# Performance work log

Hardware: AMD Instinct MI355X
Metric: run time of the kernel (lower is better)

## Reference

```python
import jax, jax.numpy as jnp
import numpy as np

KH, KW = 3, 3
PAD = 1
C_IN, C_OUT = 64, 128


def unfold(x, kh, kw, pad):
    # x: (B, C, H, W) -> (B, C, kh*kw, H*W), torch.nn.functional.unfold ordering
    B, C, H, W = x.shape
    xp = jnp.pad(x, ((0, 0), (0, 0), (pad, pad), (pad, pad)))
    patches = jnp.stack(
        [xp[:, :, i:i + H, j:j + W] for i in range(kh) for j in range(kw)],
        axis=2,
    )  # (B, C, K, H, W)
    return patches.reshape(B, C, kh * kw, H * W)


def setup_inputs() -> dict:
    key = jax.random.key(0)
    k1, k2, k3 = jax.random.split(key, 3)
    B, H, W = 8, 128, 128
    inp = jax.random.normal(k1, (B, C_IN, H, W), dtype=jnp.float32)
    g_buffer = jax.random.uniform(k2, (B, 2, H, W), dtype=jnp.float32)
    # weights param as in torch: (1, C*kh*kw, 1, out_channels), kaiming-uniform-ish
    wdepth = C_IN * KH * KW
    bound = float(np.sqrt(6.0 / wdepth))
    weights = jax.random.uniform(k3, (1, wdepth, 1, C_OUT), dtype=jnp.float32,
                                 minval=-bound, maxval=bound)
    bias = jnp.zeros((C_OUT,), dtype=jnp.float32)
    return {"input": inp, "g_buffer": g_buffer, "weights": weights, "bias": bias}


def reference(input, g_buffer, weights, bias):
    B, C, H, W = input.shape
    K = KH * KW
    L = H * W
    depth = 2.0 * (g_buffer[:, -1:, :, :] - 0.5)  # (B, 1, H, W)

    input_unf = unfold(input, KH, KW, PAD)          # (B, C, K, L)
    depth_unf = unfold(depth, KH, KW, PAD)          # (B, 1, K, L)

    # bilateral depth weighting
    dfeat = depth_unf - depth.reshape(B, 1, 1, L)   # (B, 1, K, L)
    dfeat = jnp.sum(dfeat * dfeat, axis=1)          # (B, K, L)
    wf = jnp.exp(-dfeat)
    wf = 9.0 * wf / jnp.sum(wf, axis=1, keepdims=True)  # (B, K, L)

    filt = input_unf * wf[:, None, :, :]            # (B, C, K, L)
    filt = filt.reshape(B, C * K, L)

    W2 = weights.reshape(C_OUT, C * K)              # raw reshape, matches torch .view
    out_unf = jnp.einsum('bkl,ok->bol', filt, W2)   # (B, C_OUT, L)
    out = out_unf.reshape(B, C_OUT, H, W) + bias[None, :, None, None]
    return out
```

## Files before the change

kernel.cpp:

```cpp
#include <hip/hip_runtime.h>
#include <hip/hip_bf16.h>
#include <stdint.h>

typedef _Float16 f16x8 __attribute__((ext_vector_type(8)));
typedef float    f32x4 __attribute__((ext_vector_type(4)));

#define CIN   64
#define COUT  128
#define HH    128
#define WW    128
#define BB    8

#define TROW  130
#define ROWBYTES (130 * 128)
#define TSIZE ((size_t)BB * TROW * ROWBYTES)


__global__ void prep_weights(const float* __restrict__ wflat, _Float16* __restrict__ bp) {
    int idx = blockIdx.x * 256 + threadIdx.x;
    if (idx >= 8 * 18 * 64 * 8) return;
    int j = idx & 7;
    int l = (idx >> 3) & 63;
    int s = (idx >> 9) % 18;
    int n = idx / (18 * 512);
    int o = n * 16 + (l & 15);
    int c = ((s & 1) << 5) + ((l >> 4) << 3) + j;
    int k = s >> 1;
    bp[idx] = (_Float16)wflat[o * 576 + c * 9 + k];
}

__global__ void zero_halo(_Float16* __restrict__ T) {
    int idx = blockIdx.x * 256 + threadIdx.x;
    if (idx >= 16 * 1040) return;
    int row = idx / 1040, c = idx - row * 1040;
    int b = row >> 1, yp = (row & 1) * 129;
    f16x8 z = {};
    *(f16x8*)((char*)T + (size_t)(b * TROW + yp) * ROWBYTES + c * 16) = z;
}

__global__ __launch_bounds__(256) void transpose_pass(const float* __restrict__ inp,
                                                      _Float16* __restrict__ T) {
    __shared__ float sT[64][129];
    const int b   = blockIdx.x >> 7;
    const int y   = blockIdx.x & 127;
    const int tid = threadIdx.x;

    const float* ib = inp + ((long)b * CIN * HH + y) * WW;
    const int xq = tid & 31, c8 = tid >> 5;
    #pragma unroll
    for (int i = 0; i < 8; ++i) {
        int c = c8 * 8 + i;
        float4 v = *(const float4*)(ib + (long)c * (HH * WW) + (xq << 2));
        *(float4*)&sT[c][xq << 2] = v;
    }
    __syncthreads();

    const int x  = tid & 127;
    const int ch = tid >> 7;
    char* rowp = (char*)T + (size_t)(b * TROW + y + 1) * ROWBYTES + (size_t)(x + 1) * 128;
    const int sw = (x + 1) & 7;
    for (int c0 = ch * 8; c0 < 64; c0 += 16) {
        f16x8 v;
        #pragma unroll
        for (int j = 0; j < 8; ++j) v[j] = (_Float16)sT[c0 + j][x];
        *(f16x8*)(rowp + (((c0 >> 3) ^ sw) << 4)) = v;
    }
    if (tid < 16) {
        char* basep = (char*)T + (size_t)(b * TROW + y + 1) * ROWBYTES
                    + ((tid >> 3) ? 129 * 128 : 0) + (tid & 7) * 16;
        f16x8 z = {};
        *(f16x8*)basep = z;
    }
}

__global__ __launch_bounds__(512, 2) void depthcnn_main(
    const _Float16* __restrict__ T, const float* __restrict__ gbuf,
    const float* __restrict__ bias, const _Float16* __restrict__ aprep,
    float* __restrict__ out)
{
    __shared__ __align__(1024) char sIn[4 * ROWBYTES];
    __shared__ _Float16 sWf[4][9][WW];

    const int b      = blockIdx.x >> 5;
    const int ystart = (blockIdx.x & 31) << 2;
    const int tid    = threadIdx.x;
    const int wave   = tid >> 6;
    const int lane   = tid & 63;
    const int oi     = wave >> 1;
    const int pi     = wave & 1;
    const int l15    = lane & 15;
    const int g4     = lane >> 4;
    const int pxbase = pi << 6;

    const char* Tb = (const char*)T + (size_t)b * TROW * ROWBYTES;

    #pragma unroll
    for (int i = 0; i < 3; ++i) {
        const int t = ystart + i;
        const char* src = Tb + (size_t)t * ROWBYTES;
        char* dst = sIn + (t & 3) * ROWBYTES;
        for (int c = tid; c < 1040; c += 512)
            __builtin_amdgcn_global_load_lds(
                (const __attribute__((address_space(1))) uint32_t*)(src + c * 16),
                (__attribute__((address_space(3))) uint32_t*)(dst + c * 16), 16, 0, 0);
    }

    {
        const int r = tid >> 7, x = tid & 127, y = ystart + r;
        const float* g = gbuf + ((size_t)b * 2 + 1) * (HH * WW);
        float dc = 2.f * (g[y * WW + x] - 0.5f);
        float e[9];
        float ssum = 0.f;
        #pragma unroll
        for (int k = 0; k < 9; ++k) {
            int yy = y + (k / 3) - 1;
            int xx = x + (k % 3) - 1;
            float dn = 0.f;
            if ((unsigned)yy < 128u && (unsigned)xx < 128u)
                dn = 2.f * (g[yy * WW + xx] - 0.5f);
            float df = dn - dc;
            float ek = __expf(-df * df);
            e[k] = ek;
            ssum += ek;
        }
        float sc = 9.f / ssum;
        #pragma unroll
        for (int k = 0; k < 9; ++k) sWf[r][k][x] = (_Float16)(e[k] * sc);
    }

    f16x8 afr[2][18];
    {
        const f16x8* ap = (const f16x8*)aprep;
        #pragma unroll
        for (int t2 = 0; t2 < 2; ++t2)
            #pragma unroll
            for (int s = 0; s < 18; ++s)
                afr[t2][s] = ap[(size_t)(((oi * 2 + t2) * 18) + s) * 64 + lane];
    }
    float bv[2][4];
    #pragma unroll
    for (int t2 = 0; t2 < 2; ++t2)
        #pragma unroll
        for (int r4 = 0; r4 < 4; ++r4)
            bv[t2][r4] = bias[(oi << 5) + (t2 << 4) + (g4 << 2) + r4];

    __syncthreads();

    float* ob0 = out + (size_t)b * COUT * HH * WW;

    #pragma unroll 1
    for (int r = 0; r < 4; ++r) {
        const int y = ystart + r;

        if (r < 3) {
            const int t = y + 3;
            const char* src = Tb + (size_t)t * ROWBYTES;
            char* dst = sIn + (t & 3) * ROWBYTES;
            for (int c = tid; c < 1040; c += 512)
                __builtin_amdgcn_global_load_lds(
                    (const __attribute__((address_space(1))) uint32_t*)(src + c * 16),
                    (__attribute__((address_space(3))) uint32_t*)(dst + c * 16), 16, 0, 0);
        }

        f32x4 acc[2][4];
        #pragma unroll
        for (int t2 = 0; t2 < 2; ++t2)
            #pragma unroll
            for (int pt = 0; pt < 4; ++pt)
                acc[t2][pt] = (f32x4){0.f, 0.f, 0.f, 0.f};

        #pragma unroll
        for (int s = 0; s < 18; ++s) {
            const int k  = s >> 1;
            const int ch = s & 1;
            const int dy = k / 3;
            const int dx = k - 3 * dy;
            const int slotbase = ((y + dy) & 3) * ROWBYTES;
            f16x8 bfrg[4];
            #pragma unroll
            for (int pt = 0; pt < 4; ++pt) {
                const int px = pxbase + (pt << 4) + l15;
                const int xp = px + dx;
                const int off = slotbase + (xp << 7) + ((((ch << 2) | g4) ^ (xp & 7)) << 4);
                f16x8 iv = *(const f16x8*)(sIn + off);
                _Float16 wh = sWf[r][k][px];
                f16x8 w8 = {wh, wh, wh, wh, wh, wh, wh, wh};
                bfrg[pt] = iv * w8;
            }
            #pragma unroll
            for (int t2 = 0; t2 < 2; ++t2)
                #pragma unroll
                for (int pt = 0; pt < 4; ++pt)
                    acc[t2][pt] = __builtin_amdgcn_mfma_f32_16x16x32_f16(
                        afr[t2][s], bfrg[pt], acc[t2][pt], 0, 0, 0);
        }

        __syncthreads();

        #pragma unroll
        for (int t2 = 0; t2 < 2; ++t2) {
            #pragma unroll
            for (int pt = 0; pt < 4; ++pt) {
                #pragma unroll
                for (int r4 = 0; r4 < 4; ++r4) {
                    const int o  = (oi << 5) + (t2 << 4) + (g4 << 2) + r4;
                    const int px = pxbase + (pt << 4) + l15;
                    ob0[(size_t)o * (HH * WW) + (size_t)y * WW + px] = acc[t2][pt][r4] + bv[t2][r4];
                }
            }
        }
    }
}

extern "C" void kernel_launch(void* const* d_in, const int* in_sizes, int n_in,
                              void* d_out, int out_size, void* d_ws, size_t ws_size,
                              hipStream_t stream) {
    const float* inp  = (const float*)d_in[0];
    const float* gbuf = (const float*)d_in[1];
    const float* wts  = (const float*)d_in[2];
    const float* bias = (const float*)d_in[3];

    _Float16* T  = (_Float16*)d_ws;
    _Float16* bp = (_Float16*)((char*)d_ws + TSIZE);

    hipLaunchKernelGGL(zero_halo, dim3(65), dim3(256), 0, stream, T);
    hipLaunchKernelGGL(transpose_pass, dim3(BB * HH), dim3(256), 0, stream, inp, T);
    hipLaunchKernelGGL(prep_weights, dim3(288), dim3(256), 0, stream, wts, bp);
    hipLaunchKernelGGL(depthcnn_main, dim3(256), dim3(512), 0, stream,
                       T, gbuf, bias, bp, (float*)d_out);
}
```

Baseline: 52.02 us.

## Preload all six input rows to LDS upfront and drop per-row barriers

All six halo rows a block needs are loaded into LDS in a single upfront batch, replacing the rotating four-slot ring that prefetched one row per iteration. This removes the per-iteration __syncthreads. The depth-weight table is re-laid out per pixel so each lane loads its nine weights once per row with a vector read instead of a scalar LDS read inside every MFMA step. The cost is more LDS per block and giving up the overlap of row loads with compute.

```diff
diff --git a/kernel.cpp b/kernel.cpp
--- a/kernel.cpp
+++ b/kernel.cpp
@@ -78,8 +78,8 @@
     const float* __restrict__ bias, const _Float16* __restrict__ aprep,
     float* __restrict__ out)
 {
-    __shared__ __align__(1024) char sIn[4 * ROWBYTES];
-    __shared__ _Float16 sWf[4][9][WW];
+    __shared__ __align__(1024) char sIn[6 * ROWBYTES];
+    __shared__ _Float16 sWf[4][WW][16];
 
     const int b      = blockIdx.x >> 5;
     const int ystart = (blockIdx.x & 31) << 2;
@@ -94,15 +94,12 @@
 
     const char* Tb = (const char*)T + (size_t)b * TROW * ROWBYTES;
 
-    #pragma unroll
-    for (int i = 0; i < 3; ++i) {
-        const int t = ystart + i;
-        const char* src = Tb + (size_t)t * ROWBYTES;
-        char* dst = sIn + (t & 3) * ROWBYTES;
-        for (int c = tid; c < 1040; c += 512)
+    {
+        const char* src = Tb + (size_t)ystart * ROWBYTES;
+        for (int t = tid; t < 6 * 1040; t += 512)
             __builtin_amdgcn_global_load_lds(
-                (const __attribute__((address_space(1))) uint32_t*)(src + c * 16),
-                (__attribute__((address_space(3))) uint32_t*)(dst + c * 16), 16, 0, 0);
+                (const __attribute__((address_space(1))) uint32_t*)(src + (size_t)t * 16),
+                (__attribute__((address_space(3))) uint32_t*)(sIn + t * 16), 16, 0, 0);
     }
 
     {
@@ -125,7 +122,7 @@
         }
         float sc = 9.f / ssum;
         #pragma unroll
-        for (int k = 0; k < 9; ++k) sWf[r][k][x] = (_Float16)(e[k] * sc);
+        for (int k = 0; k < 9; ++k) sWf[r][x][k] = (_Float16)(e[k] * sc);
     }
 
     f16x8 afr[2][18];
@@ -152,14 +149,13 @@
     for (int r = 0; r < 4; ++r) {
         const int y = ystart + r;
 
-        if (r < 3) {
-            const int t = y + 3;
-            const char* src = Tb + (size_t)t * ROWBYTES;
-            char* dst = sIn + (t & 3) * ROWBYTES;
-            for (int c = tid; c < 1040; c += 512)
-                __builtin_amdgcn_global_load_lds(
-                    (const __attribute__((address_space(1))) uint32_t*)(src + c * 16),
-                    (__attribute__((address_space(3))) uint32_t*)(dst + c * 16), 16, 0, 0);
+        f16x8    w07[4];
+        _Float16 w8s[4];
+        #pragma unroll
+        for (int pt = 0; pt < 4; ++pt) {
+            const int px = pxbase + (pt << 4) + l15;
+            w07[pt] = *(const f16x8*)&sWf[r][px][0];
+            w8s[pt] = sWf[r][px][8];
         }
 
         f32x4 acc[2][4];
@@ -175,15 +171,14 @@
             const int ch = s & 1;
             const int dy = k / 3;
             const int dx = k - 3 * dy;
-            const int slotbase = ((y + dy) & 3) * ROWBYTES;
+            const int rowb = (r + dy) * ROWBYTES;
             f16x8 bfrg[4];
             #pragma unroll
             for (int pt = 0; pt < 4; ++pt) {
-                const int px = pxbase + (pt << 4) + l15;
-                const int xp = px + dx;
-                const int off = slotbase + (xp << 7) + ((((ch << 2) | g4) ^ (xp & 7)) << 4);
+                const int xp  = pxbase + (pt << 4) + l15 + dx;
+                const int off = rowb + (xp << 7) + ((((ch << 2) | g4) ^ (xp & 7)) << 4);
                 f16x8 iv = *(const f16x8*)(sIn + off);
-                _Float16 wh = sWf[r][k][px];
+                _Float16 wh = (k < 8) ? w07[pt][k] : w8s[pt];
                 f16x8 w8 = {wh, wh, wh, wh, wh, wh, wh, wh};
                 bfrg[pt] = iv * w8;
             }
@@ -194,8 +189,6 @@
                     acc[t2][pt] = __builtin_amdgcn_mfma_f32_16x16x32_f16(
                         afr[t2][s], bfrg[pt], acc[t2][pt], 0, 0, 0);
         }
-
-        __syncthreads();
 
         #pragma unroll
         for (int t2 = 0; t2 < 2; ++t2) {
```

New measurement: 51.00 us. No clear change (-2.0%).
